# Kernel optimization log

Measured on AMD Instinct MI355X. Metric: run time of the kernel, lower is better.

Reference implementation:

```python
import jax, jax.numpy as jnp
import numpy as np

B, T, IN_DIM, H_DIM = 64, 512, 512, 1024


def setup_inputs() -> dict:
    key = jax.random.key(0)
    ks = jax.random.split(key, 10)
    s_in = 1.0 / np.sqrt(IN_DIM)
    s_h = 1.0 / np.sqrt(H_DIM)
    return {
        "inputs": jax.random.normal(ks[0], (B, T, IN_DIM), jnp.float32),
        "Wxr": jax.random.normal(ks[1], (H_DIM, IN_DIM), jnp.float32) * s_in,
        "bxr": jax.random.normal(ks[2], (H_DIM,), jnp.float32) * s_in,
        "Whr": jax.random.normal(ks[3], (H_DIM, H_DIM), jnp.float32) * s_h,
        "Wxz": jax.random.normal(ks[4], (H_DIM, IN_DIM), jnp.float32) * s_in,
        "bxz": jax.random.normal(ks[5], (H_DIM,), jnp.float32) * s_in,
        "Whz": jax.random.normal(ks[6], (H_DIM, H_DIM), jnp.float32) * s_h,
        "Wxn": jax.random.normal(ks[7], (H_DIM, IN_DIM), jnp.float32) * s_in,
        "bxn": jax.random.normal(ks[8], (H_DIM,), jnp.float32) * s_in,
        "Whn": jax.random.normal(ks[9], (H_DIM, H_DIM), jnp.float32) * s_h,
    }


def reference(inputs, Wxr, bxr, Whr, Wxz, bxz, Whz, Wxn, bxn, Whn):
    # Precompute all input projections in batched GEMMs: [B,T,H]
    xr = jnp.einsum("bti,hi->bth", inputs, Wxr) + bxr
    xz = jnp.einsum("bti,hi->bth", inputs, Wxz) + bxz
    xn = jnp.einsum("bti,hi->bth", inputs, Wxn) + bxn
    # time-major for scan: [T,B,H]
    xs = (xr.transpose(1, 0, 2), xz.transpose(1, 0, 2), xn.transpose(1, 0, 2))

    def step(h, x):
        xr_t, xz_t, xn_t = x
        r = jax.nn.sigmoid(xr_t + h @ Whr.T)
        z = jax.nn.sigmoid(xz_t + h @ Whz.T)
        n = jnp.tanh(xn_t + r * (h @ Whn.T))
        h_new = (1.0 - z) * n + z * h
        return h_new, h_new

    h0 = jnp.zeros((inputs.shape[0], Wxr.shape[0]), inputs.dtype)
    h_last, hs = jax.lax.scan(step, h0, xs)
    hidden_states = hs.transpose(1, 0, 2)  # [B,T,H] (batch_first)
    # dropout p=0 -> identity
    return (h_last, hidden_states)
```

## Files before the change

### kernel.cpp

```cpp
#include <hip/hip_runtime.h>

typedef __attribute__((ext_vector_type(8))) short short8;
typedef __attribute__((ext_vector_type(4))) float f32x4;
typedef __attribute__((ext_vector_type(4))) unsigned int u32x4;

#define TT 512
#define HD 1024
#define BD 64
#define NWG 256

union FRAG { u32x4 d; short8 s; };

__device__ __forceinline__ unsigned short f2bf(float f) {
  unsigned u = __float_as_uint(f);
  u += 0x7fffu + ((u >> 16) & 1u);
  return (unsigned short)(u >> 16);
}

__global__ void prep_xt(const float* __restrict__ x, short8* __restrict__ XT) {
  const int bid = blockIdx.x;
  const int b = bid >> 9;
  const int t = bid & 511;
  const int tid = threadIdx.x;
  const float* src = x + ((size_t)(b * TT + t)) * 512 + tid * 8;
  const f32x4* s4 = (const f32x4*)src;
  f32x4 lo = s4[0], hi = s4[1];
  short8 o;
#pragma unroll
  for (int j = 0; j < 4; ++j) {
    o[j] = (short)f2bf(lo[j]);
    o[4 + j] = (short)f2bf(hi[j]);
  }
  const int bt = b >> 4, m = b & 15, ks = tid >> 2, q = tid & 3;
  XT[(((size_t)bt * TT + t) * 16 + ks) * 64 + q * 16 + m] = o;
}

#define PARB ((size_t)131072)

#define WAIT_AND_LOAD()                                                   \
  asm volatile(                                                           \
      "global_load_dword %8, %10, off sc0 sc1\n\t"                        \
      "s_sleep 4\n\t"                                                     \
      "global_load_dword %9, %10, off sc0 sc1\n\t"                        \
      "1:\n\t"                                                            \
      "s_waitcnt vmcnt(1)\n\t"                                            \
      "v_cmp_gt_u32 vcc, %11, %8\n\t"                                     \
      "s_cbranch_vccz 2f\n\t"                                             \
      "global_load_dword %8, %10, off sc0 sc1\n\t"                        \
      "s_waitcnt vmcnt(1)\n\t"                                            \
      "v_cmp_gt_u32 vcc, %11, %9\n\t"                                     \
      "s_cbranch_vccz 2f\n\t"                                             \
      "global_load_dword %9, %10, off sc0 sc1\n\t"                        \
      "s_branch 1b\n\t"                                                   \
      "2:\n\t"                                                            \
      "global_load_dwordx4 %0, %12, off sc0 sc1\n\t"                      \
      "global_load_dwordx4 %1, %12, off offset:1024 sc0 sc1\n\t"          \
      "global_load_dwordx4 %2, %12, off offset:2048 sc0 sc1\n\t"          \
      "global_load_dwordx4 %3, %12, off offset:3072 sc0 sc1\n\t"          \
      "global_load_dwordx4 %4, %13, off sc0 sc1\n\t"                      \
      "global_load_dwordx4 %5, %13, off offset:1024 sc0 sc1\n\t"          \
      "global_load_dwordx4 %6, %13, off offset:2048 sc0 sc1\n\t"          \
      "global_load_dwordx4 %7, %13, off offset:3072 sc0 sc1\n\t"          \
      "s_waitcnt vmcnt(0)"                                                \
      : "=&v"(H[0]), "=&v"(H[1]), "=&v"(H[2]), "=&v"(H[3]),               \
        "=&v"(H[4]), "=&v"(H[5]), "=&v"(H[6]), "=&v"(H[7]),               \
        "=&v"(f0s), "=&v"(f1s)                                            \
      : "v"(hint_p), "v"(tt_), "v"(p0), "v"(p1)                           \
      : "vcc", "memory")

__global__ __launch_bounds__(256, 1) void gru_main(
    const float* __restrict__ Wxr, const float* __restrict__ bxr,
    const float* __restrict__ Whr,
    const float* __restrict__ Wxz, const float* __restrict__ bxz,
    const float* __restrict__ Whz,
    const float* __restrict__ Wxn, const float* __restrict__ bxn,
    const float* __restrict__ Whn,
    const short8* __restrict__ XT, char* __restrict__ HFc,
    unsigned* __restrict__ flags, float* __restrict__ out) {
  extern __shared__ char lds[];
  short8* wh = (short8*)lds;
  short8* wx = (short8*)(lds + 98304);
  float* red = (float*)(lds + 147456);

  const int wg = blockIdx.x;
  const int bt = wg & 3;
  const int ct = wg >> 2;
  const int c0 = ct << 4;
  const int tid = threadIdx.x;
  const int wv = tid >> 6;
  const int lane = tid & 63;

  for (int idx = tid; idx < 3 * 32 * 64; idx += 256) {
    const int g = idx >> 11, rem = idx & 2047, ks = rem >> 6, ln = rem & 63;
    const float* W = (g == 0) ? Whr : (g == 1) ? Whz : Whn;
    const float* src = W + (size_t)(c0 + (ln & 15)) * HD + ks * 32 + (ln >> 4) * 8;
    short8 v;
#pragma unroll
    for (int j = 0; j < 8; ++j) v[j] = (short)f2bf(src[j]);
    wh[idx] = v;
  }
  for (int idx = tid; idx < 3 * 16 * 64; idx += 256) {
    const int g = idx >> 10, rem = idx & 1023, ks = rem >> 6, ln = rem & 63;
    const float* W = (g == 0) ? Wxr : (g == 1) ? Wxz : Wxn;
    const float* src = W + (size_t)(c0 + (ln & 15)) * 512 + ks * 32 + (ln >> 4) * 8;
    short8 v;
#pragma unroll
    for (int j = 0; j < 8; ++j) v[j] = (short)f2bf(src[j]);
    wx[idx] = v;
  }
  __syncthreads();

  const int c_off = tid & 15, b_off = tid >> 4;
  const int c = c0 + c_off;
  const int b = (bt << 4) + b_off;
  const float br_ = bxr[c], bz_ = bxz[c], bn_ = bxn[c];
  float h_old = 0.f;

  const int rl = ((b_off >> 2) << 4) + c_off;
  const int rr = b_off & 3;

  const size_t prod_byte =
      ((size_t)((bt * 32 + (c >> 5)) * 64 + ((c >> 3) & 3) * 16 + b_off)) * 16 +
      (size_t)(c & 7) * 2;
  unsigned* my_flag = flags + bt * 256 + ct * 4 + wv;
  const unsigned* hint_p = flags + bt * 256 + (wv << 6) + lane;
  const char* cons_base =
      HFc + ((size_t)(bt * 32 + (wv << 3)) * 64 + lane) * 16;

  float* out_hlast = out;
  float* out_hidden = out + BD * HD;

  for (int t = 0; t < TT; ++t) {
    const char* cb = cons_base + (size_t)(t & 1) * PARB;
    const char* p0 = cb;
    const char* p1 = cb + 4096;

    const short8* xrd = XT + (((size_t)bt * TT + t) * 16 + (wv << 2)) * 64 + lane;
    short8 xa[4];
#pragma unroll
    for (int kk = 0; kk < 4; ++kk) xa[kk] = xrd[kk * 64];

    short8 whf0[8], whf1[8], whf2[8];
#pragma unroll
    for (int kk = 0; kk < 8; ++kk) {
      whf0[kk] = wh[(0 * 32 + (wv << 3) + kk) * 64 + lane];
      whf1[kk] = wh[(1 * 32 + (wv << 3) + kk) * 64 + lane];
      whf2[kk] = wh[(2 * 32 + (wv << 3) + kk) * 64 + lane];
    }

    f32x4 aR = {0.f, 0.f, 0.f, 0.f};
    f32x4 aZ = {0.f, 0.f, 0.f, 0.f};
    f32x4 aNh = {0.f, 0.f, 0.f, 0.f};
    f32x4 aNx = {0.f, 0.f, 0.f, 0.f};
#pragma unroll
    for (int kk = 0; kk < 4; ++kk) {
      const int ks = (wv << 2) + kk;
      aR = __builtin_amdgcn_mfma_f32_16x16x32_bf16(xa[kk], wx[(0 * 16 + ks) * 64 + lane], aR, 0, 0, 0);
      aZ = __builtin_amdgcn_mfma_f32_16x16x32_bf16(xa[kk], wx[(1 * 16 + ks) * 64 + lane], aZ, 0, 0, 0);
      aNx = __builtin_amdgcn_mfma_f32_16x16x32_bf16(xa[kk], wx[(2 * 16 + ks) * 64 + lane], aNx, 0, 0, 0);
    }

    u32x4 H[8];
    unsigned f0s, f1s;
    const unsigned tt_ = (unsigned)t;
    WAIT_AND_LOAD();

#pragma unroll
    for (int kk = 0; kk < 8; ++kk) {
      FRAG f;
      f.d = H[kk];
      aR = __builtin_amdgcn_mfma_f32_16x16x32_bf16(f.s, whf0[kk], aR, 0, 0, 0);
      aZ = __builtin_amdgcn_mfma_f32_16x16x32_bf16(f.s, whf1[kk], aZ, 0, 0, 0);
      aNh = __builtin_amdgcn_mfma_f32_16x16x32_bf16(f.s, whf2[kk], aNh, 0, 0, 0);
    }

    {
      f32x4* r4 = (f32x4*)red;
      r4[(0 * 4 + wv) * 64 + lane] = aR;
      r4[(1 * 4 + wv) * 64 + lane] = aZ;
      r4[(2 * 4 + wv) * 64 + lane] = aNh;
      r4[(3 * 4 + wv) * 64 + lane] = aNx;
    }
    __syncthreads();
    float sR = 0.f, sZ = 0.f, sNh = 0.f, sNx = 0.f;
#pragma unroll
    for (int v = 0; v < 4; ++v) {
      sR += red[((0 * 4 + v) * 64 + rl) * 4 + rr];
      sZ += red[((1 * 4 + v) * 64 + rl) * 4 + rr];
      sNh += red[((2 * 4 + v) * 64 + rl) * 4 + rr];
      sNx += red[((3 * 4 + v) * 64 + rl) * 4 + rr];
    }
    __syncthreads();

    const float r = 1.f / (1.f + __expf(-(sR + br_)));
    const float z = 1.f / (1.f + __expf(-(sZ + bz_)));
    float pre_n = sNx + bn_ + r * sNh;
    pre_n = fminf(fmaxf(pre_n, -30.f), 30.f);
    const float e2 = __expf(2.f * pre_n);
    const float n = (e2 - 1.f) / (e2 + 1.f);
    const float hn = (1.f - z) * n + z * h_old;
    h_old = hn;

    const unsigned hb = f2bf(hn);
    const unsigned hb_hi = (unsigned)__shfl_down((int)hb, 1);

    if (t < TT - 1) {
      if (!(c_off & 1)) {
        __hip_atomic_store(
            (unsigned*)(HFc + (size_t)((t + 1) & 1) * PARB + prod_byte),
            hb | (hb_hi << 16), __ATOMIC_RELAXED, __HIP_MEMORY_SCOPE_AGENT);
      }
      asm volatile("s_waitcnt vmcnt(0)" ::: "memory");
      if (lane == 0) {
        __hip_atomic_store(my_flag, (unsigned)(t + 1), __ATOMIC_RELAXED,
                           __HIP_MEMORY_SCOPE_AGENT);
      }
      out_hidden[((size_t)b * TT + t) * HD + c] = hn;
    } else {
      out_hidden[((size_t)b * TT + t) * HD + c] = hn;
      out_hlast[(size_t)b * HD + c] = hn;
    }
  }
}

extern "C" void kernel_launch(void* const* d_in, const int* in_sizes, int n_in,
                              void* d_out, int out_size, void* d_ws, size_t ws_size,
                              hipStream_t stream) {
  const float* inputs = (const float*)d_in[0];
  const float* Wxr = (const float*)d_in[1];
  const float* bxr = (const float*)d_in[2];
  const float* Whr = (const float*)d_in[3];
  const float* Wxz = (const float*)d_in[4];
  const float* bxz = (const float*)d_in[5];
  const float* Whz = (const float*)d_in[6];
  const float* Wxn = (const float*)d_in[7];
  const float* bxn = (const float*)d_in[8];
  const float* Whn = (const float*)d_in[9];
  float* out = (float*)d_out;

  char* ws = (char*)d_ws;
  short8* XT = (short8*)ws;
  char* HF = ws + 33554432;
  unsigned* flags = (unsigned*)(ws + 33554432 + 262144);

  hipMemsetAsync(HF, 0, 262144 + 4096, stream);
  prep_xt<<<dim3(64 * 512), dim3(64), 0, stream>>>(inputs, XT);

  (void)hipFuncSetAttribute((const void*)gru_main,
                            hipFuncAttributeMaxDynamicSharedMemorySize, 163840);
  gru_main<<<dim3(NWG), dim3(256), 163840, stream>>>(
      Wxr, bxr, Whr, Wxz, bxz, Whz, Wxn, bxn, Whn, XT, HF, flags, out);
}
```

Measured before the change: 1.513 ms.

## Keep GRU weight fragments in registers and double-buffer the LDS reduction

Weight fragments (both recurrent and input projections) are loaded once from global memory, converted to bf16 and held in VGPRs for the whole sequence. This removes the per-timestep LDS reads of weight fragments. The reduction buffer is double-buffered by timestep parity, which drops the second __syncthreads per step. The cost is high register pressure (36 short8 fragments per lane), which risks spills, and the dynamic LDS request shrinks.

```diff
diff --git a/kernel.cpp b/kernel.cpp
--- a/kernel.cpp
+++ b/kernel.cpp
@@ -15,6 +15,18 @@
   unsigned u = __float_as_uint(f);
   u += 0x7fffu + ((u >> 16) & 1u);
   return (unsigned short)(u >> 16);
+}
+
+__device__ __forceinline__ short8 ld_bf8(const float* s) {
+  const f32x4* s4 = (const f32x4*)s;
+  f32x4 lo = s4[0], hi = s4[1];
+  short8 o;
+#pragma unroll
+  for (int j = 0; j < 4; ++j) {
+    o[j] = (short)f2bf(lo[j]);
+    o[4 + j] = (short)f2bf(hi[j]);
+  }
+  return o;
 }
 
 __global__ void prep_xt(const float* __restrict__ x, short8* __restrict__ XT) {
@@ -22,15 +34,7 @@
   const int b = bid >> 9;
   const int t = bid & 511;
   const int tid = threadIdx.x;
-  const float* src = x + ((size_t)(b * TT + t)) * 512 + tid * 8;
-  const f32x4* s4 = (const f32x4*)src;
-  f32x4 lo = s4[0], hi = s4[1];
-  short8 o;
-#pragma unroll
-  for (int j = 0; j < 4; ++j) {
-    o[j] = (short)f2bf(lo[j]);
-    o[4 + j] = (short)f2bf(hi[j]);
-  }
+  short8 o = ld_bf8(x + ((size_t)(b * TT + t)) * 512 + tid * 8);
   const int bt = b >> 4, m = b & 15, ks = tid >> 2, q = tid & 3;
   XT[(((size_t)bt * TT + t) * 16 + ks) * 64 + q * 16 + m] = o;
 }
@@ -78,9 +82,7 @@
     const short8* __restrict__ XT, char* __restrict__ HFc,
     unsigned* __restrict__ flags, float* __restrict__ out) {
   extern __shared__ char lds[];
-  short8* wh = (short8*)lds;
-  short8* wx = (short8*)(lds + 98304);
-  float* red = (float*)(lds + 147456);
+  float* red = (float*)lds;
 
   const int wg = blockIdx.x;
   const int bt = wg & 3;
@@ -90,25 +92,25 @@
   const int wv = tid >> 6;
   const int lane = tid & 63;
 
-  for (int idx = tid; idx < 3 * 32 * 64; idx += 256) {
-    const int g = idx >> 11, rem = idx & 2047, ks = rem >> 6, ln = rem & 63;
-    const float* W = (g == 0) ? Whr : (g == 1) ? Whz : Whn;
-    const float* src = W + (size_t)(c0 + (ln & 15)) * HD + ks * 32 + (ln >> 4) * 8;
-    short8 v;
-#pragma unroll
-    for (int j = 0; j < 8; ++j) v[j] = (short)f2bf(src[j]);
-    wh[idx] = v;
+  short8 whr_[8], whz_[8], whn_[8], wxr_[4], wxz_[4], wxn_[4];
+  {
+    const size_t bc = (size_t)(c0 + (lane & 15));
+    const int ko = (lane >> 4) * 8;
+#pragma unroll
+    for (int kk = 0; kk < 8; ++kk) {
+      const int ks = (wv << 3) + kk;
+      whr_[kk] = ld_bf8(Whr + bc * HD + ks * 32 + ko);
+      whz_[kk] = ld_bf8(Whz + bc * HD + ks * 32 + ko);
+      whn_[kk] = ld_bf8(Whn + bc * HD + ks * 32 + ko);
+    }
+#pragma unroll
+    for (int kk = 0; kk < 4; ++kk) {
+      const int ks = (wv << 2) + kk;
+      wxr_[kk] = ld_bf8(Wxr + bc * 512 + ks * 32 + ko);
+      wxz_[kk] = ld_bf8(Wxz + bc * 512 + ks * 32 + ko);
+      wxn_[kk] = ld_bf8(Wxn + bc * 512 + ks * 32 + ko);
+    }
   }
-  for (int idx = tid; idx < 3 * 16 * 64; idx += 256) {
-    const int g = idx >> 10, rem = idx & 1023, ks = rem >> 6, ln = rem & 63;
-    const float* W = (g == 0) ? Wxr : (g == 1) ? Wxz : Wxn;
-    const float* src = W + (size_t)(c0 + (ln & 15)) * 512 + ks * 32 + (ln >> 4) * 8;
-    short8 v;
-#pragma unroll
-    for (int j = 0; j < 8; ++j) v[j] = (short)f2bf(src[j]);
-    wx[idx] = v;
-  }
-  __syncthreads();
 
   const int c_off = tid & 15, b_off = tid >> 4;
   const int c = c0 + c_off;
@@ -140,24 +142,15 @@
 #pragma unroll
     for (int kk = 0; kk < 4; ++kk) xa[kk] = xrd[kk * 64];
 
-    short8 whf0[8], whf1[8], whf2[8];
-#pragma unroll
-    for (int kk = 0; kk < 8; ++kk) {
-      whf0[kk] = wh[(0 * 32 + (wv << 3) + kk) * 64 + lane];
-      whf1[kk] = wh[(1 * 32 + (wv << 3) + kk) * 64 + lane];
-      whf2[kk] = wh[(2 * 32 + (wv << 3) + kk) * 64 + lane];
-    }
-
     f32x4 aR = {0.f, 0.f, 0.f, 0.f};
     f32x4 aZ = {0.f, 0.f, 0.f, 0.f};
     f32x4 aNh = {0.f, 0.f, 0.f, 0.f};
     f32x4 aNx = {0.f, 0.f, 0.f, 0.f};
 #pragma unroll
     for (int kk = 0; kk < 4; ++kk) {
-      const int ks = (wv << 2) + kk;
-      aR = __builtin_amdgcn_mfma_f32_16x16x32_bf16(xa[kk], wx[(0 * 16 + ks) * 64 + lane], aR, 0, 0, 0);
-      aZ = __builtin_amdgcn_mfma_f32_16x16x32_bf16(xa[kk], wx[(1 * 16 + ks) * 64 + lane], aZ, 0, 0, 0);
-      aNx = __builtin_amdgcn_mfma_f32_16x16x32_bf16(xa[kk], wx[(2 * 16 + ks) * 64 + lane], aNx, 0, 0, 0);
+      aR = __builtin_amdgcn_mfma_f32_16x16x32_bf16(xa[kk], wxr_[kk], aR, 0, 0, 0);
+      aZ = __builtin_amdgcn_mfma_f32_16x16x32_bf16(xa[kk], wxz_[kk], aZ, 0, 0, 0);
+      aNx = __builtin_amdgcn_mfma_f32_16x16x32_bf16(xa[kk], wxn_[kk], aNx, 0, 0, 0);
     }
 
     u32x4 H[8];
@@ -169,13 +162,14 @@
     for (int kk = 0; kk < 8; ++kk) {
       FRAG f;
       f.d = H[kk];
-      aR = __builtin_amdgcn_mfma_f32_16x16x32_bf16(f.s, whf0[kk], aR, 0, 0, 0);
-      aZ = __builtin_amdgcn_mfma_f32_16x16x32_bf16(f.s, whf1[kk], aZ, 0, 0, 0);
-      aNh = __builtin_amdgcn_mfma_f32_16x16x32_bf16(f.s, whf2[kk], aNh, 0, 0, 0);
-    }
-
+      aR = __builtin_amdgcn_mfma_f32_16x16x32_bf16(f.s, whr_[kk], aR, 0, 0, 0);
+      aZ = __builtin_amdgcn_mfma_f32_16x16x32_bf16(f.s, whz_[kk], aZ, 0, 0, 0);
+      aNh = __builtin_amdgcn_mfma_f32_16x16x32_bf16(f.s, whn_[kk], aNh, 0, 0, 0);
+    }
+
+    float* redb = red + (t & 1) * (4 * 4 * 64 * 4);
     {
-      f32x4* r4 = (f32x4*)red;
+      f32x4* r4 = (f32x4*)redb;
       r4[(0 * 4 + wv) * 64 + lane] = aR;
       r4[(1 * 4 + wv) * 64 + lane] = aZ;
       r4[(2 * 4 + wv) * 64 + lane] = aNh;
@@ -185,12 +179,11 @@
     float sR = 0.f, sZ = 0.f, sNh = 0.f, sNx = 0.f;
 #pragma unroll
     for (int v = 0; v < 4; ++v) {
-      sR += red[((0 * 4 + v) * 64 + rl) * 4 + rr];
-      sZ += red[((1 * 4 + v) * 64 + rl) * 4 + rr];
-      sNh += red[((2 * 4 + v) * 64 + rl) * 4 + rr];
-      sNx += red[((3 * 4 + v) * 64 + rl) * 4 + rr];
-    }
-    __syncthreads();
+      sR += redb[((0 * 4 + v) * 64 + rl) * 4 + rr];
+      sZ += redb[((1 * 4 + v) * 64 + rl) * 4 + rr];
+      sNh += redb[((2 * 4 + v) * 64 + rl) * 4 + rr];
+      sNx += redb[((3 * 4 + v) * 64 + rl) * 4 + rr];
+    }
 
     const float r = 1.f / (1.f + __expf(-(sR + br_)));
     const float z = 1.f / (1.f + __expf(-(sZ + bz_)));
@@ -247,7 +240,7 @@
   prep_xt<<<dim3(64 * 512), dim3(64), 0, stream>>>(inputs, XT);
 
   (void)hipFuncSetAttribute((const void*)gru_main,
-                            hipFuncAttributeMaxDynamicSharedMemorySize, 163840);
-  gru_main<<<dim3(NWG), dim3(256), 163840, stream>>>(
+                            hipFuncAttributeMaxDynamicSharedMemorySize, 98304);
+  gru_main<<<dim3(NWG), dim3(256), 98304, stream>>>(
       Wxr, bxr, Whr, Wxz, bxz, Whz, Wxn, bxn, Whn, XT, HF, flags, out);
 }
```

Result: slower. 1.955 ms (+29.2%).
